# Performance work log

Hardware: AMD Instinct MI355X
Metric: run time of the kernel (lower is better)

## Reference

```python
import jax, jax.numpy as jnp
import numpy as np

RES = 0.5  # voxels.resolution
N_VOX = 65536
M_PTS = 2048


def quaternion_matrix(quat, tran):
    # quat normalized with sqrt(2/|q|^2), then 4x4 outer product Q = q q^T
    q = quat * jnp.sqrt(2.0 / jnp.sum(quat ** 2))
    Q = jnp.outer(q, q)
    R = jnp.array([
        [1.0 - Q[2, 2] - Q[3, 3], Q[1, 2] - Q[3, 0],       Q[1, 3] + Q[2, 0],       tran[0]],
        [Q[1, 2] + Q[3, 0],       1.0 - Q[1, 1] - Q[3, 3], Q[2, 3] - Q[1, 0],       tran[1]],
        [Q[1, 3] - Q[2, 0],       Q[2, 3] + Q[1, 0],       1.0 - Q[1, 1] - Q[2, 2], tran[2]],
        [0.0,                     0.0,                     0.0,                     1.0]],
        dtype=quat.dtype)
    return R


def setup_inputs() -> dict:
    key = jax.random.key(0)
    ks = jax.random.split(key, 8)
    quat = jax.random.normal(ks[0], (4,), jnp.float32)
    tran = jax.random.normal(ks[1], (3,), jnp.float32) * 0.1
    model = jax.random.normal(ks[2], (M_PTS, 3), jnp.float32) * 0.5
    view_matrix = jnp.eye(4, dtype=jnp.float32) + 0.05 * jax.random.normal(ks[3], (4, 4), jnp.float32)
    centers = jax.random.uniform(ks[4], (N_VOX, 3), jnp.float32, -1.0, 1.0)
    free = jax.random.uniform(ks[5], (N_VOX,), jnp.float32)
    occupied_by_other = jax.random.uniform(ks[6], (N_VOX,), jnp.float32)
    masks = (jax.random.uniform(ks[7], (N_VOX,), jnp.float32) < 0.3).astype(jnp.float32)
    return {"quat": quat, "tran": tran, "model": model, "view_matrix": view_matrix,
            "centers": centers, "free": free, "occupied_by_other": occupied_by_other,
            "masks": masks}


def reference(quat, tran, model, view_matrix, centers, free, occupied_by_other, masks):
    mat_eye = quaternion_matrix(quat, tran)                       # (4,4)
    mat_world = jnp.linalg.inv(view_matrix) @ mat_eye             # (4,4)
    model_h = jnp.concatenate([model, jnp.ones((model.shape[0], 1), model.dtype)], 1).T  # (4,M)
    pred = mat_world @ model_h                                    # (4,M)
    pred = (pred / pred[3])[:3].T                                 # (M,3)

    # pairwise distances in voxel coordinates: ||(pred - center)/RES||
    c = centers / RES                                             # (N,3)
    p = pred / RES                                                # (M,3)
    d2 = (jnp.sum(c * c, axis=1)[:, None]
          + jnp.sum(p * p, axis=1)[None, :]
          - 2.0 * (c @ p.T))                                      # (N,M)
    dmin = jnp.sqrt(jnp.maximum(jnp.min(d2, axis=1), 0.0))        # (N,)
    dmin = jnp.minimum(dmin, RES / 2.0)                           # clamp max
    # occupand > 0 write, else stays 0 -> relu (occupand is already >= 0)
    occupied_by_pred = jnp.maximum(1.0 - dmin / (RES / 2.0), 0.0)

    pred_sum = occupied_by_pred.sum()
    mask_sum = masks.sum()
    t1 = jnp.where(pred_sum > 0,
                   ((free + occupied_by_other) * occupied_by_pred).sum()
                   / jnp.where(pred_sum > 0, pred_sum, 1.0), 0.0)
    t2 = jnp.where(mask_sum > 0,
                   (masks * occupied_by_pred).sum()
                   / jnp.where(mask_sum > 0, mask_sum, 1.0), 0.0)
    return t1 - t2
```

## Files before the change

### kernel.cpp

```cpp
#include <hip/hip_runtime.h>
#include <math.h>

#define M_PTS   2048
#define N_VOX   65536
#define VPT     4
#define VPB     256
#define NBLK    (N_VOX / VPB)
#define NWAVES  16
#define CHUNK   (M_PTS / NWAVES)


__global__ __launch_bounds__(1024) void k_fused(const float* __restrict__ quat,
                                                const float* __restrict__ tran,
                                                const float* __restrict__ model,
                                                const float* __restrict__ view,
                                                const float* __restrict__ centers,
                                                const float* __restrict__ freev,
                                                const float* __restrict__ occ_other,
                                                const float* __restrict__ masks,
                                                float* __restrict__ partial) {
    __shared__ float4 sp[M_PTS];
    __shared__ float  pmin[NWAVES * VPB];
    __shared__ float  sred[16];

    const int tid = threadIdx.x;

    float W[16];
    {
        float q0 = quat[0], q1 = quat[1], q2 = quat[2], q3 = quat[3];
        float nq = q0*q0 + q1*q1 + q2*q2 + q3*q3;
        float s = sqrtf(2.0f / nq);
        q0 *= s; q1 *= s; q2 *= s; q3 *= s;
        float E[16];
        E[0]  = 1.0f - q2*q2 - q3*q3; E[1]  = q1*q2 - q3*q0;        E[2]  = q1*q3 + q2*q0;        E[3]  = tran[0];
        E[4]  = q1*q2 + q3*q0;        E[5]  = 1.0f - q1*q1 - q3*q3; E[6]  = q2*q3 - q1*q0;        E[7]  = tran[1];
        E[8]  = q1*q3 - q2*q0;        E[9]  = q2*q3 + q1*q0;        E[10] = 1.0f - q1*q1 - q2*q2; E[11] = tran[2];
        E[12] = 0.0f; E[13] = 0.0f; E[14] = 0.0f; E[15] = 1.0f;

        float m[16], inv[16];
        #pragma unroll
        for (int i = 0; i < 16; i++) m[i] = view[i];

        inv[0]  =  m[5]*m[10]*m[15] - m[5]*m[11]*m[14] - m[9]*m[6]*m[15] + m[9]*m[7]*m[14] + m[13]*m[6]*m[11] - m[13]*m[7]*m[10];
        inv[4]  = -m[4]*m[10]*m[15] + m[4]*m[11]*m[14] + m[8]*m[6]*m[15] - m[8]*m[7]*m[14] - m[12]*m[6]*m[11] + m[12]*m[7]*m[10];
        inv[8]  =  m[4]*m[9]*m[15]  - m[4]*m[11]*m[13] - m[8]*m[5]*m[15] + m[8]*m[7]*m[13] + m[12]*m[5]*m[11] - m[12]*m[7]*m[9];
        inv[12] = -m[4]*m[9]*m[14]  + m[4]*m[10]*m[13] + m[8]*m[5]*m[14] - m[8]*m[6]*m[13] - m[12]*m[5]*m[10] + m[12]*m[6]*m[9];
        inv[1]  = -m[1]*m[10]*m[15] + m[1]*m[11]*m[14] + m[9]*m[2]*m[15] - m[9]*m[3]*m[14] - m[13]*m[2]*m[11] + m[13]*m[3]*m[10];
        inv[5]  =  m[0]*m[10]*m[15] - m[0]*m[11]*m[14] - m[8]*m[2]*m[15] + m[8]*m[3]*m[14] + m[12]*m[2]*m[11] - m[12]*m[3]*m[10];
        inv[9]  = -m[0]*m[9]*m[15]  + m[0]*m[11]*m[13] + m[8]*m[1]*m[15] - m[8]*m[3]*m[13] - m[12]*m[1]*m[11] + m[12]*m[3]*m[9];
        inv[13] =  m[0]*m[9]*m[14]  - m[0]*m[10]*m[13] - m[8]*m[1]*m[14] + m[8]*m[2]*m[13] + m[12]*m[1]*m[10] - m[12]*m[2]*m[9];
        inv[2]  =  m[1]*m[6]*m[15]  - m[1]*m[7]*m[14]  - m[5]*m[2]*m[15] + m[5]*m[3]*m[14] + m[13]*m[2]*m[7]  - m[13]*m[3]*m[6];
        inv[6]  = -m[0]*m[6]*m[15]  + m[0]*m[7]*m[14]  + m[4]*m[2]*m[15] - m[4]*m[3]*m[14] - m[12]*m[2]*m[7]  + m[12]*m[3]*m[6];
        inv[10] =  m[0]*m[5]*m[15]  - m[0]*m[7]*m[13]  - m[4]*m[1]*m[15] + m[4]*m[3]*m[13] + m[12]*m[1]*m[7]  - m[12]*m[3]*m[5];
        inv[14] = -m[0]*m[5]*m[14]  + m[0]*m[6]*m[13]  + m[4]*m[1]*m[14] - m[4]*m[2]*m[13] - m[12]*m[1]*m[6]  + m[12]*m[2]*m[5];
        inv[3]  = -m[1]*m[6]*m[11]  + m[1]*m[7]*m[10]  + m[5]*m[2]*m[11] - m[5]*m[3]*m[10] - m[9]*m[2]*m[7]   + m[9]*m[3]*m[6];
        inv[7]  =  m[0]*m[6]*m[11]  - m[0]*m[7]*m[10]  - m[4]*m[2]*m[11] + m[4]*m[3]*m[10] + m[8]*m[2]*m[7]   - m[8]*m[3]*m[6];
        inv[11] = -m[0]*m[5]*m[11]  + m[0]*m[7]*m[9]   + m[4]*m[1]*m[11] - m[4]*m[3]*m[9]  - m[8]*m[1]*m[7]   + m[8]*m[3]*m[5];
        inv[15] =  m[0]*m[5]*m[10]  - m[0]*m[6]*m[9]   - m[4]*m[1]*m[10] + m[4]*m[2]*m[9]  + m[8]*m[1]*m[6]   - m[8]*m[2]*m[5];

        float det = m[0]*inv[0] + m[1]*inv[4] + m[2]*inv[8] + m[3]*inv[12];
        float rdet = 1.0f / det;

        #pragma unroll
        for (int r = 0; r < 4; r++) {
            #pragma unroll
            for (int c = 0; c < 4; c++) {
                float a = 0.0f;
                #pragma unroll
                for (int k = 0; k < 4; k++) a += inv[4*r+k] * rdet * E[4*k+c];
                W[4*r+c] = a;
            }
        }
    }

    #pragma unroll
    for (int i = tid; i < M_PTS; i += 1024) {
        float x = model[3*i + 0];
        float y = model[3*i + 1];
        float z = model[3*i + 2];
        float X  = W[0]*x + W[1]*y + W[2]*z  + W[3];
        float Y  = W[4]*x + W[5]*y + W[6]*z  + W[7];
        float Z  = W[8]*x + W[9]*y + W[10]*z + W[11];
        float Wd = W[12]*x + W[13]*y + W[14]*z + W[15];
        float rw = 2.0f / Wd;
        float px = X * rw, py = Y * rw, pz = Z * rw;
        float h  = 0.5f * (px*px + py*py + pz*pz);
        sp[i] = make_float4(px, py, pz, h);
    }
    __syncthreads();

    const int lane = tid & 63;
    const int wave = tid >> 6;
    const int vbase = blockIdx.x * VPB + lane * VPT;

    float nx[VPT], ny[VPT], nz[VPT], mm[VPT];
    #pragma unroll
    for (int k = 0; k < VPT; k++) {
        int g = vbase + k;
        nx[k] = -centers[3*g + 0] * 2.0f;
        ny[k] = -centers[3*g + 1] * 2.0f;
        nz[k] = -centers[3*g + 2] * 2.0f;
        mm[k] = 1e30f;
    }

    const float4* base = sp + wave * CHUNK;
    #pragma unroll 4
    for (int j = 0; j < CHUNK; ++j) {
        float4 p = base[j];
        #pragma unroll
        for (int k = 0; k < VPT; k++)
            mm[k] = fminf(mm[k], fmaf(nx[k], p.x, fmaf(ny[k], p.y, fmaf(nz[k], p.z, p.w))));
    }
    #pragma unroll
    for (int k = 0; k < VPT; k++)
        pmin[wave * VPB + lane * VPT + k] = mm[k];
    __syncthreads();

    if (tid < VPB) {
        const int g = blockIdx.x * VPB + tid;
        float m = 1e30f;
        #pragma unroll
        for (int c = 0; c < NWAVES; c++)
            m = fminf(m, pmin[c * VPB + tid]);
        float cx = centers[3*g + 0] * 2.0f;
        float cy = centers[3*g + 1] * 2.0f;
        float cz = centers[3*g + 2] * 2.0f;
        float c2 = cx*cx + cy*cy + cz*cz;
        float d2 = fmaf(2.0f, m, c2);
        float dmin = fminf(sqrtf(fmaxf(d2, 0.0f)), 0.25f);
        float occ  = fmaxf(1.0f - 4.0f * dmin, 0.0f);

        float mk = masks[g];
        float v0 = occ;
        float v1 = (freev[g] + occ_other[g]) * occ;
        float v2 = mk * occ;
        float v3 = mk;

        #pragma unroll
        for (int off = 32; off > 0; off >>= 1) {
            v0 += __shfl_down(v0, off);
            v1 += __shfl_down(v1, off);
            v2 += __shfl_down(v2, off);
            v3 += __shfl_down(v3, off);
        }
        if (lane == 0) {
            sred[wave*4 + 0] = v0;
            sred[wave*4 + 1] = v1;
            sred[wave*4 + 2] = v2;
            sred[wave*4 + 3] = v3;
        }
    }
    __syncthreads();
    if (tid < 4) {
        float s = sred[tid] + sred[4 + tid] + sred[8 + tid] + sred[12 + tid];
        partial[blockIdx.x * 4 + tid] = s;
    }
}

__global__ __launch_bounds__(256) void k_final(const float* __restrict__ partial,
                                               float* __restrict__ out) {
    __shared__ float sred[16];
    const int tid  = threadIdx.x;
    const int lane = tid & 63;
    const int wave = tid >> 6;

    float4 p = ((const float4*)partial)[tid];
    float v0 = p.x, v1 = p.y, v2 = p.z, v3 = p.w;

    #pragma unroll
    for (int off = 32; off > 0; off >>= 1) {
        v0 += __shfl_down(v0, off);
        v1 += __shfl_down(v1, off);
        v2 += __shfl_down(v2, off);
        v3 += __shfl_down(v3, off);
    }
    if (lane == 0) {
        sred[wave*4 + 0] = v0;
        sred[wave*4 + 1] = v1;
        sred[wave*4 + 2] = v2;
        sred[wave*4 + 3] = v3;
    }
    __syncthreads();
    if (tid == 0) {
        float ps = sred[0] + sred[4] + sred[8]  + sred[12];
        float fo = sred[1] + sred[5] + sred[9]  + sred[13];
        float mo = sred[2] + sred[6] + sred[10] + sred[14];
        float ms = sred[3] + sred[7] + sred[11] + sred[15];
        float t1 = (ps > 0.0f) ? (fo / ps) : 0.0f;
        float t2 = (ms > 0.0f) ? (mo / ms) : 0.0f;
        out[0] = t1 - t2;
    }
}

extern "C" void kernel_launch(void* const* d_in, const int* in_sizes, int n_in,
                              void* d_out, int out_size, void* d_ws, size_t ws_size,
                              hipStream_t stream) {
    const float* quat      = (const float*)d_in[0];
    const float* tran      = (const float*)d_in[1];
    const float* model     = (const float*)d_in[2];
    const float* view      = (const float*)d_in[3];
    const float* centers   = (const float*)d_in[4];
    const float* freev     = (const float*)d_in[5];
    const float* occ_other = (const float*)d_in[6];
    const float* masks     = (const float*)d_in[7];
    float* out     = (float*)d_out;
    float* partial = (float*)d_ws;

    k_fused<<<NBLK, 1024, 0, stream>>>(quat, tran, model, view, centers, freev,
                                       occ_other, masks, partial);
    k_final<<<1, 256, 0, stream>>>(partial, out);
}
```

Baseline: 83.16 us.

## Precompute transformed points in separate kernel and stream them via scalar loads

Splits the point transform into a small prep kernel that writes transformed points to workspace, so each main block no longer recomputes the 4x4 inverse and transforms all points into LDS. The main kernel reads the points with wave-uniform s_load_dwordx4 through inline asm, so the values land in scalar registers and feed the FMAs directly instead of going through LDS reads. The final reduction kernel is replaced by atomics and a last-block ticket. This adds an extra launch and atomic contention, and the inline asm waits on all eight loads before each batch, which may stall.

Result: slower. 146.3 us (+75.9%).

```diff
diff --git a/kernel.cpp b/kernel.cpp
--- a/kernel.cpp
+++ b/kernel.cpp
@@ -9,88 +9,102 @@
 #define NWAVES  16
 #define CHUNK   (M_PTS / NWAVES)
 
-
-__global__ __launch_bounds__(1024) void k_fused(const float* __restrict__ quat,
-                                                const float* __restrict__ tran,
-                                                const float* __restrict__ model,
-                                                const float* __restrict__ view,
-                                                const float* __restrict__ centers,
-                                                const float* __restrict__ freev,
-                                                const float* __restrict__ occ_other,
-                                                const float* __restrict__ masks,
-                                                float* __restrict__ partial) {
-    __shared__ float4 sp[M_PTS];
-    __shared__ float  pmin[NWAVES * VPB];
-    __shared__ float  sred[16];
-
-    const int tid = threadIdx.x;
-
+typedef float f4v __attribute__((ext_vector_type(4)));
+
+
+__device__ __forceinline__ void compute_W(const float* __restrict__ quat,
+                                          const float* __restrict__ tran,
+                                          const float* __restrict__ view,
+                                          float* W) {
+    float q0 = quat[0], q1 = quat[1], q2 = quat[2], q3 = quat[3];
+    float nq = q0*q0 + q1*q1 + q2*q2 + q3*q3;
+    float s = sqrtf(2.0f / nq);
+    q0 *= s; q1 *= s; q2 *= s; q3 *= s;
+    float E[16];
+    E[0]  = 1.0f - q2*q2 - q3*q3; E[1]  = q1*q2 - q3*q0;        E[2]  = q1*q3 + q2*q0;        E[3]  = tran[0];
+    E[4]  = q1*q2 + q3*q0;        E[5]  = 1.0f - q1*q1 - q3*q3; E[6]  = q2*q3 - q1*q0;        E[7]  = tran[1];
+    E[8]  = q1*q3 - q2*q0;        E[9]  = q2*q3 + q1*q0;        E[10] = 1.0f - q1*q1 - q2*q2; E[11] = tran[2];
+    E[12] = 0.0f; E[13] = 0.0f; E[14] = 0.0f; E[15] = 1.0f;
+
+    float m[16], inv[16];
+    #pragma unroll
+    for (int i = 0; i < 16; i++) m[i] = view[i];
+
+    inv[0]  =  m[5]*m[10]*m[15] - m[5]*m[11]*m[14] - m[9]*m[6]*m[15] + m[9]*m[7]*m[14] + m[13]*m[6]*m[11] - m[13]*m[7]*m[10];
+    inv[4]  = -m[4]*m[10]*m[15] + m[4]*m[11]*m[14] + m[8]*m[6]*m[15] - m[8]*m[7]*m[14] - m[12]*m[6]*m[11] + m[12]*m[7]*m[10];
+    inv[8]  =  m[4]*m[9]*m[15]  - m[4]*m[11]*m[13] - m[8]*m[5]*m[15] + m[8]*m[7]*m[13] + m[12]*m[5]*m[11] - m[12]*m[7]*m[9];
+    inv[12] = -m[4]*m[9]*m[14]  + m[4]*m[10]*m[13] + m[8]*m[5]*m[14] - m[8]*m[6]*m[13] - m[12]*m[5]*m[10] + m[12]*m[6]*m[9];
+    inv[1]  = -m[1]*m[10]*m[15] + m[1]*m[11]*m[14] + m[9]*m[2]*m[15] - m[9]*m[3]*m[14] - m[13]*m[2]*m[11] + m[13]*m[3]*m[10];
+    inv[5]  =  m[0]*m[10]*m[15] - m[0]*m[11]*m[14] - m[8]*m[2]*m[15] + m[8]*m[3]*m[14] + m[12]*m[2]*m[11] - m[12]*m[3]*m[10];
+    inv[9]  = -m[0]*m[9]*m[15]  + m[0]*m[11]*m[13] + m[8]*m[1]*m[15] - m[8]*m[3]*m[13] - m[12]*m[1]*m[11] + m[12]*m[3]*m[9];
+    inv[13] =  m[0]*m[9]*m[14]  - m[0]*m[10]*m[13] - m[8]*m[1]*m[14] + m[8]*m[2]*m[13] + m[12]*m[1]*m[10] - m[12]*m[2]*m[9];
+    inv[2]  =  m[1]*m[6]*m[15]  - m[1]*m[7]*m[14]  - m[5]*m[2]*m[15] + m[5]*m[3]*m[14] + m[13]*m[2]*m[7]  - m[13]*m[3]*m[6];
+    inv[6]  = -m[0]*m[6]*m[15]  + m[0]*m[7]*m[14]  + m[4]*m[2]*m[15] - m[4]*m[3]*m[14] - m[12]*m[2]*m[7]  + m[12]*m[3]*m[6];
+    inv[10] =  m[0]*m[5]*m[15]  - m[0]*m[7]*m[13]  - m[4]*m[1]*m[15] + m[4]*m[3]*m[13] + m[12]*m[1]*m[7]  - m[12]*m[3]*m[5];
+    inv[14] = -m[0]*m[5]*m[14]  + m[0]*m[6]*m[13]  + m[4]*m[1]*m[14] - m[4]*m[2]*m[13] - m[12]*m[1]*m[6]  + m[12]*m[2]*m[5];
+    inv[3]  = -m[1]*m[6]*m[11]  + m[1]*m[7]*m[10]  + m[5]*m[2]*m[11] - m[5]*m[3]*m[10] - m[9]*m[2]*m[7]   + m[9]*m[3]*m[6];
+    inv[7]  =  m[0]*m[6]*m[11]  - m[0]*m[7]*m[10]  - m[4]*m[2]*m[11] + m[4]*m[3]*m[10] + m[8]*m[2]*m[7]   - m[8]*m[3]*m[6];
+    inv[11] = -m[0]*m[5]*m[11]  + m[0]*m[7]*m[9]   + m[4]*m[1]*m[11] - m[4]*m[3]*m[9]  - m[8]*m[1]*m[7]   + m[8]*m[3]*m[5];
+    inv[15] =  m[0]*m[5]*m[10]  - m[0]*m[6]*m[9]   - m[4]*m[1]*m[10] + m[4]*m[2]*m[9]  + m[8]*m[1]*m[6]   - m[8]*m[2]*m[5];
+
+    float det = m[0]*inv[0] + m[1]*inv[4] + m[2]*inv[8] + m[3]*inv[12];
+    float rdet = 1.0f / det;
+
+    #pragma unroll
+    for (int r = 0; r < 4; r++) {
+        #pragma unroll
+        for (int c = 0; c < 4; c++) {
+            float a = 0.0f;
+            #pragma unroll
+            for (int k = 0; k < 4; k++) a += inv[4*r+k] * rdet * E[4*k+c];
+            W[4*r+c] = a;
+        }
+    }
+}
+
+__global__ __launch_bounds__(256) void k_prep(const float* __restrict__ quat,
+                                              const float* __restrict__ tran,
+                                              const float* __restrict__ model,
+                                              const float* __restrict__ view,
+                                              float4* __restrict__ pts,
+                                              float* __restrict__ acc,
+                                              int* __restrict__ ticket) {
     float W[16];
-    {
-        float q0 = quat[0], q1 = quat[1], q2 = quat[2], q3 = quat[3];
-        float nq = q0*q0 + q1*q1 + q2*q2 + q3*q3;
-        float s = sqrtf(2.0f / nq);
-        q0 *= s; q1 *= s; q2 *= s; q3 *= s;
-        float E[16];
-        E[0]  = 1.0f - q2*q2 - q3*q3; E[1]  = q1*q2 - q3*q0;        E[2]  = q1*q3 + q2*q0;        E[3]  = tran[0];
-        E[4]  = q1*q2 + q3*q0;        E[5]  = 1.0f - q1*q1 - q3*q3; E[6]  = q2*q3 - q1*q0;        E[7]  = tran[1];
-        E[8]  = q1*q3 - q2*q0;        E[9]  = q2*q3 + q1*q0;        E[10] = 1.0f - q1*q1 - q2*q2; E[11] = tran[2];
-        E[12] = 0.0f; E[13] = 0.0f; E[14] = 0.0f; E[15] = 1.0f;
-
-        float m[16], inv[16];
-        #pragma unroll
-        for (int i = 0; i < 16; i++) m[i] = view[i];
-
-        inv[0]  =  m[5]*m[10]*m[15] - m[5]*m[11]*m[14] - m[9]*m[6]*m[15] + m[9]*m[7]*m[14] + m[13]*m[6]*m[11] - m[13]*m[7]*m[10];
-        inv[4]  = -m[4]*m[10]*m[15] + m[4]*m[11]*m[14] + m[8]*m[6]*m[15] - m[8]*m[7]*m[14] - m[12]*m[6]*m[11] + m[12]*m[7]*m[10];
-        inv[8]  =  m[4]*m[9]*m[15]  - m[4]*m[11]*m[13] - m[8]*m[5]*m[15] + m[8]*m[7]*m[13] + m[12]*m[5]*m[11] - m[12]*m[7]*m[9];
-        inv[12] = -m[4]*m[9]*m[14]  + m[4]*m[10]*m[13] + m[8]*m[5]*m[14] - m[8]*m[6]*m[13] - m[12]*m[5]*m[10] + m[12]*m[6]*m[9];
-        inv[1]  = -m[1]*m[10]*m[15] + m[1]*m[11]*m[14] + m[9]*m[2]*m[15] - m[9]*m[3]*m[14] - m[13]*m[2]*m[11] + m[13]*m[3]*m[10];
-        inv[5]  =  m[0]*m[10]*m[15] - m[0]*m[11]*m[14] - m[8]*m[2]*m[15] + m[8]*m[3]*m[14] + m[12]*m[2]*m[11] - m[12]*m[3]*m[10];
-        inv[9]  = -m[0]*m[9]*m[15]  + m[0]*m[11]*m[13] + m[8]*m[1]*m[15] - m[8]*m[3]*m[13] - m[12]*m[1]*m[11] + m[12]*m[3]*m[9];
-        inv[13] =  m[0]*m[9]*m[14]  - m[0]*m[10]*m[13] - m[8]*m[1]*m[14] + m[8]*m[2]*m[13] + m[12]*m[1]*m[10] - m[12]*m[2]*m[9];
-        inv[2]  =  m[1]*m[6]*m[15]  - m[1]*m[7]*m[14]  - m[5]*m[2]*m[15] + m[5]*m[3]*m[14] + m[13]*m[2]*m[7]  - m[13]*m[3]*m[6];
-        inv[6]  = -m[0]*m[6]*m[15]  + m[0]*m[7]*m[14]  + m[4]*m[2]*m[15] - m[4]*m[3]*m[14] - m[12]*m[2]*m[7]  + m[12]*m[3]*m[6];
-        inv[10] =  m[0]*m[5]*m[15]  - m[0]*m[7]*m[13]  - m[4]*m[1]*m[15] + m[4]*m[3]*m[13] + m[12]*m[1]*m[7]  - m[12]*m[3]*m[5];
-        inv[14] = -m[0]*m[5]*m[14]  + m[0]*m[6]*m[13]  + m[4]*m[1]*m[14] - m[4]*m[2]*m[13] - m[12]*m[1]*m[6]  + m[12]*m[2]*m[5];
-        inv[3]  = -m[1]*m[6]*m[11]  + m[1]*m[7]*m[10]  + m[5]*m[2]*m[11] - m[5]*m[3]*m[10] - m[9]*m[2]*m[7]   + m[9]*m[3]*m[6];
-        inv[7]  =  m[0]*m[6]*m[11]  - m[0]*m[7]*m[10]  - m[4]*m[2]*m[11] + m[4]*m[3]*m[10] + m[8]*m[2]*m[7]   - m[8]*m[3]*m[6];
-        inv[11] = -m[0]*m[5]*m[11]  + m[0]*m[7]*m[9]   + m[4]*m[1]*m[11] - m[4]*m[3]*m[9]  - m[8]*m[1]*m[7]   + m[8]*m[3]*m[5];
-        inv[15] =  m[0]*m[5]*m[10]  - m[0]*m[6]*m[9]   - m[4]*m[1]*m[10] + m[4]*m[2]*m[9]  + m[8]*m[1]*m[6]   - m[8]*m[2]*m[5];
-
-        float det = m[0]*inv[0] + m[1]*inv[4] + m[2]*inv[8] + m[3]*inv[12];
-        float rdet = 1.0f / det;
-
-        #pragma unroll
-        for (int r = 0; r < 4; r++) {
-            #pragma unroll
-            for (int c = 0; c < 4; c++) {
-                float a = 0.0f;
-                #pragma unroll
-                for (int k = 0; k < 4; k++) a += inv[4*r+k] * rdet * E[4*k+c];
-                W[4*r+c] = a;
-            }
-        }
-    }
-
-    #pragma unroll
-    for (int i = tid; i < M_PTS; i += 1024) {
-        float x = model[3*i + 0];
-        float y = model[3*i + 1];
-        float z = model[3*i + 2];
-        float X  = W[0]*x + W[1]*y + W[2]*z  + W[3];
-        float Y  = W[4]*x + W[5]*y + W[6]*z  + W[7];
-        float Z  = W[8]*x + W[9]*y + W[10]*z + W[11];
-        float Wd = W[12]*x + W[13]*y + W[14]*z + W[15];
-        float rw = 2.0f / Wd;
-        float px = X * rw, py = Y * rw, pz = Z * rw;
-        float h  = 0.5f * (px*px + py*py + pz*pz);
-        sp[i] = make_float4(px, py, pz, h);
-    }
-    __syncthreads();
-
+    compute_W(quat, tran, view, W);
+
+    const int i = blockIdx.x * 256 + threadIdx.x;
+    float x = model[3*i + 0];
+    float y = model[3*i + 1];
+    float z = model[3*i + 2];
+    float X  = W[0]*x + W[1]*y + W[2]*z  + W[3];
+    float Y  = W[4]*x + W[5]*y + W[6]*z  + W[7];
+    float Z  = W[8]*x + W[9]*y + W[10]*z + W[11];
+    float Wd = W[12]*x + W[13]*y + W[14]*z + W[15];
+    float rw = 2.0f / Wd;
+    float px = X * rw, py = Y * rw, pz = Z * rw;
+    float h  = 0.5f * (px*px + py*py + pz*pz);
+    pts[i] = make_float4(px, py, pz, h);
+
+    if (blockIdx.x == 0 && threadIdx.x == 0) {
+        acc[0] = 0.0f; acc[1] = 0.0f; acc[2] = 0.0f; acc[3] = 0.0f;
+        *ticket = 0;
+    }
+}
+
+__global__ __launch_bounds__(1024) void k_main(const float* __restrict__ ws_pts,
+                                               const float* __restrict__ centers,
+                                               const float* __restrict__ freev,
+                                               const float* __restrict__ occ_other,
+                                               const float* __restrict__ masks,
+                                               float* __restrict__ acc,
+                                               int* __restrict__ ticket,
+                                               float* __restrict__ out) {
+    __shared__ float pmin[NWAVES * VPB];
+    __shared__ float sred[16];
+
+    const int tid  = threadIdx.x;
     const int lane = tid & 63;
-    const int wave = tid >> 6;
+    const int wave_u = __builtin_amdgcn_readfirstlane(tid >> 6);
     const int vbase = blockIdx.x * VPB + lane * VPT;
 
     float nx[VPT], ny[VPT], nz[VPT], mm[VPT];
@@ -103,17 +117,41 @@
         mm[k] = 1e30f;
     }
 
-    const float4* base = sp + wave * CHUNK;
-    #pragma unroll 4
-    for (int j = 0; j < CHUNK; ++j) {
-        float4 p = base[j];
-        #pragma unroll
-        for (int k = 0; k < VPT; k++)
-            mm[k] = fminf(mm[k], fmaf(nx[k], p.x, fmaf(ny[k], p.y, fmaf(nz[k], p.z, p.w))));
-    }
+    const f4v* base = (const f4v*)ws_pts + wave_u * CHUNK;
+
+    for (int jb = 0; jb < CHUNK; jb += 8) {
+        const f4v* bp = base + jb;
+        f4v P0, P1, P2, P3, P4, P5, P6, P7;
+        asm volatile(
+            "s_load_dwordx4 %0, %8, 0x00\n\t"
+            "s_load_dwordx4 %1, %8, 0x10\n\t"
+            "s_load_dwordx4 %2, %8, 0x20\n\t"
+            "s_load_dwordx4 %3, %8, 0x30\n\t"
+            "s_load_dwordx4 %4, %8, 0x40\n\t"
+            "s_load_dwordx4 %5, %8, 0x50\n\t"
+            "s_load_dwordx4 %6, %8, 0x60\n\t"
+            "s_load_dwordx4 %7, %8, 0x70\n\t"
+            "s_waitcnt lgkmcnt(0)"
+            : "=&s"(P0), "=&s"(P1), "=&s"(P2), "=&s"(P3),
+              "=&s"(P4), "=&s"(P5), "=&s"(P6), "=&s"(P7)
+            : "s"(bp));
+
+        #define DO_PT(P)                                                            \
+        {                                                                           \
+            float hv = (P).w;                                                       \
+            _Pragma("unroll")                                                       \
+            for (int k = 0; k < VPT; k++)                                           \
+                mm[k] = fminf(mm[k],                                                \
+                    fmaf(nx[k], (P).x, fmaf(ny[k], (P).y, fmaf(nz[k], (P).z, hv))));\
+        }
+        DO_PT(P0) DO_PT(P1) DO_PT(P2) DO_PT(P3)
+        DO_PT(P4) DO_PT(P5) DO_PT(P6) DO_PT(P7)
+        #undef DO_PT
+    }
+
     #pragma unroll
     for (int k = 0; k < VPT; k++)
-        pmin[wave * VPB + lane * VPT + k] = mm[k];
+        pmin[wave_u * VPB + lane * VPT + k] = mm[k];
     __syncthreads();
 
     if (tid < VPB) {
@@ -144,51 +182,31 @@
             v3 += __shfl_down(v3, off);
         }
         if (lane == 0) {
-            sred[wave*4 + 0] = v0;
-            sred[wave*4 + 1] = v1;
-            sred[wave*4 + 2] = v2;
-            sred[wave*4 + 3] = v3;
+            sred[wave_u*4 + 0] = v0;
+            sred[wave_u*4 + 1] = v1;
+            sred[wave_u*4 + 2] = v2;
+            sred[wave_u*4 + 3] = v3;
         }
     }
     __syncthreads();
+
     if (tid < 4) {
         float s = sred[tid] + sred[4 + tid] + sred[8 + tid] + sred[12 + tid];
-        partial[blockIdx.x * 4 + tid] = s;
-    }
-}
-
-__global__ __launch_bounds__(256) void k_final(const float* __restrict__ partial,
-                                               float* __restrict__ out) {
-    __shared__ float sred[16];
-    const int tid  = threadIdx.x;
-    const int lane = tid & 63;
-    const int wave = tid >> 6;
-
-    float4 p = ((const float4*)partial)[tid];
-    float v0 = p.x, v1 = p.y, v2 = p.z, v3 = p.w;
-
-    #pragma unroll
-    for (int off = 32; off > 0; off >>= 1) {
-        v0 += __shfl_down(v0, off);
-        v1 += __shfl_down(v1, off);
-        v2 += __shfl_down(v2, off);
-        v3 += __shfl_down(v3, off);
-    }
-    if (lane == 0) {
-        sred[wave*4 + 0] = v0;
-        sred[wave*4 + 1] = v1;
-        sred[wave*4 + 2] = v2;
-        sred[wave*4 + 3] = v3;
-    }
-    __syncthreads();
+        atomicAdd(&acc[tid], s);
+    }
+    __threadfence();
     if (tid == 0) {
-        float ps = sred[0] + sred[4] + sred[8]  + sred[12];
-        float fo = sred[1] + sred[5] + sred[9]  + sred[13];
-        float mo = sred[2] + sred[6] + sred[10] + sred[14];
-        float ms = sred[3] + sred[7] + sred[11] + sred[15];
-        float t1 = (ps > 0.0f) ? (fo / ps) : 0.0f;
-        float t2 = (ms > 0.0f) ? (mo / ms) : 0.0f;
-        out[0] = t1 - t2;
+        int old = atomicAdd(ticket, 1);
+        if (old == NBLK - 1) {
+            __threadfence();
+            float ps = atomicAdd(&acc[0], 0.0f);
+            float fo = atomicAdd(&acc[1], 0.0f);
+            float mo = atomicAdd(&acc[2], 0.0f);
+            float ms = atomicAdd(&acc[3], 0.0f);
+            float t1 = (ps > 0.0f) ? (fo / ps) : 0.0f;
+            float t2 = (ms > 0.0f) ? (mo / ms) : 0.0f;
+            out[0] = t1 - t2;
+        }
     }
 }
 
@@ -203,10 +221,14 @@
     const float* freev     = (const float*)d_in[5];
     const float* occ_other = (const float*)d_in[6];
     const float* masks     = (const float*)d_in[7];
-    float* out     = (float*)d_out;
-    float* partial = (float*)d_ws;
-
-    k_fused<<<NBLK, 1024, 0, stream>>>(quat, tran, model, view, centers, freev,
-                                       occ_other, masks, partial);
-    k_final<<<1, 256, 0, stream>>>(partial, out);
-}
+    float* out = (float*)d_out;
+    float* wsf = (float*)d_ws;
+
+    float4* pts   = (float4*)wsf;
+    float*  acc   = wsf + 8192;
+    int*    ticket= (int*)(wsf + 8196);
+
+    k_prep<<<M_PTS / 256, 256, 0, stream>>>(quat, tran, model, view, pts, acc, ticket);
+    k_main<<<NBLK, 1024, 0, stream>>>(wsf, centers, freev, occ_other, masks,
+                                      acc, ticket, out);
+}
```
